# Optimization experiments

Hardware: AMD Instinct MI355X
Metric: run time of the kernel (lower is better)

## Reference

```python
import jax, jax.numpy as jnp
import numpy as np

NUM_ATOMS = 512
NUM_DIMS = 128
H = 32
W = 32
B = 32


def make_dct_dict():
    # rows i: cos((2n+1) * i * pi / (2*num_dims)), L2-normalized; Dict = weights.T -> [D, A]
    i = jnp.arange(NUM_ATOMS, dtype=jnp.float32)[:, None]
    n = jnp.arange(NUM_DIMS, dtype=jnp.float32)[None, :]
    atoms = jnp.cos((2.0 * n + 1.0) * i * (np.pi / (2.0 * NUM_DIMS)))  # [A, D]
    atoms = atoms / jnp.linalg.norm(atoms, axis=1, keepdims=True)
    return atoms.T  # [D, A]


def setup_inputs() -> dict:
    key = jax.random.key(0)
    x = jax.random.normal(key, (B, NUM_DIMS, H, W), dtype=jnp.float32)
    Dict = make_dct_dict()                      # [D, A] learned param (DCT init)
    L = jnp.sum(Dict ** 2)                      # ||Dict||_F^2 (scalar param)
    alpha = jnp.ones((1, H, W, 1), dtype=jnp.float32)  # learned threshold param
    return {"x": x, "Dict": Dict, "alpha": alpha, "L": L, "num_iters": 16}


def reference(x, Dict, alpha, L, num_iters):
    l = alpha / L                                # [1,H,W,1] threshold, broadcasts over atoms
    xt = jnp.transpose(x, (0, 2, 3, 1))          # [B,H,W,D]
    S = (jnp.eye(NUM_ATOMS, dtype=Dict.dtype) - (Dict.T @ Dict) / L).T  # [A,A]
    y = xt @ Dict                                # [B,H,W,A]

    def soft_thresh(v):
        return jnp.sign(v) * jnp.maximum(jnp.abs(v) - l, 0.0)

    z = soft_thresh(y)

    def body(z, _):
        z = soft_thresh(z @ S + y / L)
        return z, None

    z, _ = jax.lax.scan(body, z, None, length=num_iters)
    x_recon = z @ Dict.T                         # [B,H,W,D]
    return (jnp.transpose(z, (0, 3, 1, 2)),      # [B,A,H,W]
            jnp.transpose(x_recon, (0, 3, 1, 2)),  # [B,D,H,W]
            Dict)
```

## Files before the change

### kernel.cpp

```cpp
#include <hip/hip_runtime.h>
#include <hip/hip_bf16.h>

typedef __bf16 bf16_t;
typedef bf16_t bf16x8 __attribute__((ext_vector_type(8)));
typedef float f32x4 __attribute__((ext_vector_type(4)));
typedef unsigned short u16;
typedef unsigned int u32;

static __device__ __forceinline__ u16 f2bf(float f) {
    __hip_bfloat16 h = __float2bfloat16(f);
    return __builtin_bit_cast(u16, h);
}
static __device__ __forceinline__ bf16_t fb(float f) {
    return __builtin_bit_cast(bf16_t, f2bf(f));
}
static __device__ __forceinline__ float bf2f(u16 u) {
    u32 x = ((u32)u) << 16;
    return __builtin_bit_cast(float, x);
}
static __device__ __forceinline__ float softthr(float v, float l) {
    return copysignf(fmaxf(fabsf(v) - l, 0.0f), v);
}

__global__ __launch_bounds__(256) void copy_dict(const float* __restrict__ Dict,
                                                 float* __restrict__ outd)
{
    int i = blockIdx.x * 256 + threadIdx.x;
    outd[i] = Dict[i];
}

__global__ __launch_bounds__(512, 2)
void lista_main(const float* __restrict__ x,
                const float* __restrict__ Dict,
                const float* __restrict__ alpha,
                const float* __restrict__ Lp,
                const int* __restrict__ nip,
                float* __restrict__ outz,
                float* __restrict__ outr)
{
    __shared__ __align__(16) u16 zl[32 * 512];
    __shared__ __align__(16) u16 rl[32 * 128];
    __shared__ __align__(16) u16 xs[32 * 128];
    __shared__ __align__(16) u16 pb[32 * 4 * 128];

    const int t = threadIdx.x;
    const int lane = t & 63;
    const int l15 = lane & 15;
    const int lg = lane >> 4;
    const int wave = t >> 6;
    const int dg = wave >> 2;
    const int ag = wave & 3;
    const int atb = wave << 6;
    const int bb = blockIdx.x >> 5;
    const int hw0 = (blockIdx.x & 31) << 5;
    const float invL = 1.0f / Lp[0];
    const int niter = nip[0];

    const int rpx = t & 31;
    const int roc = t >> 5;

    for (int i = t; i < 32 * 128; i += 512) {
        int d = i >> 5, px = i & 31;
        xs[((px << 7) + d) ^ ((px & 7) << 3)] =
            f2bf(x[((bb * 128 + d) << 10) + hw0 + px]);
    }

    float thr[2];
#pragma unroll
    for (int nt = 0; nt < 2; ++nt)
        thr[nt] = alpha[hw0 + nt * 16 + l15] * invL;

    bf16x8 g1a[4][4];
#pragma unroll
    for (int mt = 0; mt < 4; ++mt) {
        const float* drow = Dict + ((dg * 64 + mt * 16 + l15) << 9) + ag * 128 + lg * 8;
#pragma unroll
        for (int kt = 0; kt < 4; ++kt) {
            f32x4 c0 = *reinterpret_cast<const f32x4*>(drow + kt * 32);
            f32x4 c1 = *reinterpret_cast<const f32x4*>(drow + kt * 32 + 4);
#pragma unroll
            for (int j = 0; j < 4; ++j) {
                g1a[mt][kt][j] = fb(-c0[j]);
                g1a[mt][kt][j + 4] = fb(-c1[j]);
            }
        }
    }
    bf16x8 g2a[4][4];
#pragma unroll
    for (int at = 0; at < 4; ++at)
#pragma unroll
        for (int kt = 0; kt < 4; ++kt)
#pragma unroll
            for (int j = 0; j < 8; ++j)
                g2a[at][kt][j] = fb(Dict[((kt * 32 + lg * 8 + j) << 9) + atb + at * 16 + l15]);

    __syncthreads();

    f32x4 accz[4][2];
#pragma unroll
    for (int at = 0; at < 4; ++at)
#pragma unroll
        for (int nt = 0; nt < 2; ++nt)
            accz[at][nt] = f32x4{0.f, 0.f, 0.f, 0.f};

    auto run_g2 = [&](const u16* __restrict__ bsrc) {
#pragma unroll
        for (int kt = 0; kt < 4; ++kt) {
            bf16x8 Bf[2];
#pragma unroll
            for (int nt = 0; nt < 2; ++nt) {
                int px = nt * 16 + l15;
                Bf[nt] = *reinterpret_cast<const bf16x8*>(
                    &bsrc[((px << 7) + kt * 32 + lg * 8) ^ ((px & 7) << 3)]);
            }
            __builtin_amdgcn_s_setprio(1);
#pragma unroll
            for (int at = 0; at < 4; ++at)
#pragma unroll
                for (int nt = 0; nt < 2; ++nt)
                    accz[at][nt] = __builtin_amdgcn_mfma_f32_16x16x32_bf16(
                        g2a[at][kt], Bf[nt], accz[at][nt], 0, 0, 0);
            __builtin_amdgcn_s_setprio(0);
        }
#pragma unroll
        for (int at = 0; at < 4; ++at)
#pragma unroll
            for (int nt = 0; nt < 2; ++nt) {
                int px = nt * 16 + l15;
                f32x4 a = accz[at][nt];
                a[0] = softthr(a[0], thr[nt]);
                a[1] = softthr(a[1], thr[nt]);
                a[2] = softthr(a[2], thr[nt]);
                a[3] = softthr(a[3], thr[nt]);
                accz[at][nt] = a;
                uint2 pk;
                pk.x = (u32)f2bf(a[0]) | ((u32)f2bf(a[1]) << 16);
                pk.y = (u32)f2bf(a[2]) | ((u32)f2bf(a[3]) << 16);
                *reinterpret_cast<uint2*>(
                    &zl[((px << 9) + atb + at * 16 + lg * 4) ^ ((px & 7) << 3)]) = pk;
            }
    };

    auto run_g1 = [&]() {
        f32x4 a1p[4][2];
#pragma unroll
        for (int mt = 0; mt < 4; ++mt)
#pragma unroll
            for (int nt = 0; nt < 2; ++nt)
                a1p[mt][nt] = f32x4{0.f, 0.f, 0.f, 0.f};
#pragma unroll
        for (int kt = 0; kt < 4; ++kt) {
            bf16x8 Bf[2];
#pragma unroll
            for (int nt = 0; nt < 2; ++nt) {
                int px = nt * 16 + l15;
                Bf[nt] = *reinterpret_cast<const bf16x8*>(
                    &zl[((px << 9) + ag * 128 + kt * 32 + lg * 8) ^ ((px & 7) << 3)]);
            }
            __builtin_amdgcn_s_setprio(1);
#pragma unroll
            for (int mt = 0; mt < 4; ++mt)
#pragma unroll
                for (int nt = 0; nt < 2; ++nt)
                    a1p[mt][nt] = __builtin_amdgcn_mfma_f32_16x16x32_bf16(
                        g1a[mt][kt], Bf[nt], a1p[mt][nt], 0, 0, 0);
            __builtin_amdgcn_s_setprio(0);
        }
#pragma unroll
        for (int mt = 0; mt < 4; ++mt)
#pragma unroll
            for (int nt = 0; nt < 2; ++nt) {
                int px = nt * 16 + l15;
                int d0 = dg * 64 + mt * 16 + lg * 4;
                f32x4 a = a1p[mt][nt];
                uint2 pk;
                pk.x = (u32)f2bf(a[0]) | ((u32)f2bf(a[1]) << 16);
                pk.y = (u32)f2bf(a[2]) | ((u32)f2bf(a[3]) << 16);
                *reinterpret_cast<uint2*>(
                    &pb[((px << 9) + (ag << 7) + d0) ^ ((px & 7) << 3)]) = pk;
            }
    };

    run_g2(xs);
    __syncthreads();

    for (int it = 1; it <= niter; ++it) {
        run_g1();
        __syncthreads();
        {
            const int sw = (rpx & 7) << 3;
            bf16x8 p0 = *reinterpret_cast<const bf16x8*>(&pb[((rpx << 9) + 0 * 128 + roc * 8) ^ sw]);
            bf16x8 p1 = *reinterpret_cast<const bf16x8*>(&pb[((rpx << 9) + 1 * 128 + roc * 8) ^ sw]);
            bf16x8 p2 = *reinterpret_cast<const bf16x8*>(&pb[((rpx << 9) + 2 * 128 + roc * 8) ^ sw]);
            bf16x8 p3 = *reinterpret_cast<const bf16x8*>(&pb[((rpx << 9) + 3 * 128 + roc * 8) ^ sw]);
            bf16x8 xv = *reinterpret_cast<const bf16x8*>(&xs[((rpx << 7) + roc * 8) ^ sw]);
            bf16x8 rv;
#pragma unroll
            for (int e = 0; e < 8; ++e) {
                float s = ((float)xv[e] + (float)p0[e]) + ((float)p1[e] + (float)p2[e]) + (float)p3[e];
                rv[e] = fb(s * invL);
            }
            *reinterpret_cast<bf16x8*>(&rl[((rpx << 7) + roc * 8) ^ sw]) = rv;
        }
        __syncthreads();
        run_g2(rl);
        __syncthreads();
    }

    run_g1();
    __syncthreads();
    float rec[8];
    {
        const int sw = (rpx & 7) << 3;
        bf16x8 p0 = *reinterpret_cast<const bf16x8*>(&pb[((rpx << 9) + 0 * 128 + roc * 8) ^ sw]);
        bf16x8 p1 = *reinterpret_cast<const bf16x8*>(&pb[((rpx << 9) + 1 * 128 + roc * 8) ^ sw]);
        bf16x8 p2 = *reinterpret_cast<const bf16x8*>(&pb[((rpx << 9) + 2 * 128 + roc * 8) ^ sw]);
        bf16x8 p3 = *reinterpret_cast<const bf16x8*>(&pb[((rpx << 9) + 3 * 128 + roc * 8) ^ sw]);
#pragma unroll
        for (int e = 0; e < 8; ++e)
            rec[e] = -(((float)p0[e] + (float)p1[e]) + ((float)p2[e] + (float)p3[e]));
    }

    for (int i = t; i < 32 * 512; i += 512) {
        int a = i >> 5, px = i & 31;
        float zv = bf2f(zl[((px << 9) + a) ^ ((px & 7) << 3)]);
        __builtin_nontemporal_store(zv, &outz[((bb * 512 + a) << 10) + hw0 + px]);
    }
    __syncthreads();

    {
        float* wf = reinterpret_cast<float*>(pb);
        const int swf = (rpx & 7) << 2;
        f32x4 lo{rec[0], rec[1], rec[2], rec[3]};
        f32x4 hi{rec[4], rec[5], rec[6], rec[7]};
        *reinterpret_cast<f32x4*>(&wf[((rpx << 7) + roc * 8) ^ swf]) = lo;
        *reinterpret_cast<f32x4*>(&wf[((rpx << 7) + roc * 8 + 4) ^ swf]) = hi;
    }
    __syncthreads();

    {
        const float* wf = reinterpret_cast<const float*>(pb);
        for (int i = t; i < 32 * 128; i += 512) {
            int d = i >> 5, px = i & 31;
            __builtin_nontemporal_store(wf[((px << 7) + d) ^ ((px & 7) << 2)],
                                        &outr[((bb * 128 + d) << 10) + hw0 + px]);
        }
    }
}

extern "C" void kernel_launch(void* const* d_in, const int* in_sizes, int n_in,
                              void* d_out, int out_size, void* d_ws, size_t ws_size,
                              hipStream_t stream)
{
    const float* x     = (const float*)d_in[0];
    const float* Dict  = (const float*)d_in[1];
    const float* alpha = (const float*)d_in[2];
    const float* Lp    = (const float*)d_in[3];
    const int*   nip   = (const int*)d_in[4];

    float* outz = (float*)d_out;
    float* outr = outz + 32 * 512 * 1024;
    float* outd = outr + 32 * 128 * 1024;

    copy_dict<<<dim3(256), dim3(256), 0, stream>>>(Dict, outd);
    lista_main<<<dim3(1024), dim3(512), 0, stream>>>(x, Dict, alpha, Lp, nip,
                                                     outz, outr);
}
```

Measured before the change: 213.6 us.

## Double pixels per block to 64 and split the reconstruction GEMM K two ways

```diff
diff --git a/kernel.cpp b/kernel.cpp
--- a/kernel.cpp
+++ b/kernel.cpp
@@ -18,8 +18,8 @@
     u32 x = ((u32)u) << 16;
     return __builtin_bit_cast(float, x);
 }
-static __device__ __forceinline__ float softthr(float v, float l) {
-    return copysignf(fmaxf(fabsf(v) - l, 0.0f), v);
+static __device__ __forceinline__ float softthr(float v, float l, float nl) {
+    return v - fmaxf(nl, fminf(v, l));
 }
 
 __global__ __launch_bounds__(256) void copy_dict(const float* __restrict__ Dict,
@@ -38,44 +38,43 @@
                 float* __restrict__ outz,
                 float* __restrict__ outr)
 {
-    __shared__ __align__(16) u16 zl[32 * 512];
-    __shared__ __align__(16) u16 rl[32 * 128];
-    __shared__ __align__(16) u16 xs[32 * 128];
-    __shared__ __align__(16) u16 pb[32 * 4 * 128];
+    __shared__ __align__(16) u16 zl[64 * 512];
+    __shared__ __align__(16) u16 rl[64 * 128];
+    __shared__ __align__(16) u16 xs[64 * 128];
+    __shared__ __align__(16) u16 pb[64 * 256];
 
     const int t = threadIdx.x;
     const int lane = t & 63;
     const int l15 = lane & 15;
     const int lg = lane >> 4;
     const int wave = t >> 6;
-    const int dg = wave >> 2;
-    const int ag = wave & 3;
+    const int dg = wave >> 1;
+    const int ag = wave & 1;
     const int atb = wave << 6;
-    const int bb = blockIdx.x >> 5;
-    const int hw0 = (blockIdx.x & 31) << 5;
+    const int bb = blockIdx.x >> 4;
+    const int hw0 = (blockIdx.x & 15) << 6;
     const float invL = 1.0f / Lp[0];
     const int niter = nip[0];
 
-    const int rpx = t & 31;
-    const int roc = t >> 5;
-
-    for (int i = t; i < 32 * 128; i += 512) {
-        int d = i >> 5, px = i & 31;
+    for (int i = t; i < 64 * 128; i += 512) {
+        int d = i >> 6, px = i & 63;
         xs[((px << 7) + d) ^ ((px & 7) << 3)] =
             f2bf(x[((bb * 128 + d) << 10) + hw0 + px]);
     }
 
-    float thr[2];
-#pragma unroll
-    for (int nt = 0; nt < 2; ++nt)
+    float thr[4], nthr[4];
+#pragma unroll
+    for (int nt = 0; nt < 4; ++nt) {
         thr[nt] = alpha[hw0 + nt * 16 + l15] * invL;
-
-    bf16x8 g1a[4][4];
-#pragma unroll
-    for (int mt = 0; mt < 4; ++mt) {
-        const float* drow = Dict + ((dg * 64 + mt * 16 + l15) << 9) + ag * 128 + lg * 8;
-#pragma unroll
-        for (int kt = 0; kt < 4; ++kt) {
+        nthr[nt] = -thr[nt];
+    }
+
+    bf16x8 g1a[2][8];
+#pragma unroll
+    for (int mt = 0; mt < 2; ++mt) {
+        const float* drow = Dict + ((dg * 32 + mt * 16 + l15) << 9) + ag * 256 + lg * 8;
+#pragma unroll
+        for (int kt = 0; kt < 8; ++kt) {
             f32x4 c0 = *reinterpret_cast<const f32x4*>(drow + kt * 32);
             f32x4 c1 = *reinterpret_cast<const f32x4*>(drow + kt * 32 + 4);
 #pragma unroll
@@ -96,42 +95,40 @@
 
     __syncthreads();
 
-    f32x4 accz[4][2];
+    f32x4 accz[4][4];
 #pragma unroll
     for (int at = 0; at < 4; ++at)
 #pragma unroll
-        for (int nt = 0; nt < 2; ++nt)
+        for (int nt = 0; nt < 4; ++nt)
             accz[at][nt] = f32x4{0.f, 0.f, 0.f, 0.f};
 
     auto run_g2 = [&](const u16* __restrict__ bsrc) {
 #pragma unroll
         for (int kt = 0; kt < 4; ++kt) {
-            bf16x8 Bf[2];
-#pragma unroll
-            for (int nt = 0; nt < 2; ++nt) {
+            bf16x8 Bf[4];
+#pragma unroll
+            for (int nt = 0; nt < 4; ++nt) {
                 int px = nt * 16 + l15;
                 Bf[nt] = *reinterpret_cast<const bf16x8*>(
                     &bsrc[((px << 7) + kt * 32 + lg * 8) ^ ((px & 7) << 3)]);
             }
-            __builtin_amdgcn_s_setprio(1);
 #pragma unroll
             for (int at = 0; at < 4; ++at)
 #pragma unroll
-                for (int nt = 0; nt < 2; ++nt)
+                for (int nt = 0; nt < 4; ++nt)
                     accz[at][nt] = __builtin_amdgcn_mfma_f32_16x16x32_bf16(
                         g2a[at][kt], Bf[nt], accz[at][nt], 0, 0, 0);
-            __builtin_amdgcn_s_setprio(0);
         }
 #pragma unroll
         for (int at = 0; at < 4; ++at)
 #pragma unroll
-            for (int nt = 0; nt < 2; ++nt) {
+            for (int nt = 0; nt < 4; ++nt) {
                 int px = nt * 16 + l15;
                 f32x4 a = accz[at][nt];
-                a[0] = softthr(a[0], thr[nt]);
-                a[1] = softthr(a[1], thr[nt]);
-                a[2] = softthr(a[2], thr[nt]);
-                a[3] = softthr(a[3], thr[nt]);
+                a[0] = softthr(a[0], thr[nt], nthr[nt]);
+                a[1] = softthr(a[1], thr[nt], nthr[nt]);
+                a[2] = softthr(a[2], thr[nt], nthr[nt]);
+                a[3] = softthr(a[3], thr[nt], nthr[nt]);
                 accz[at][nt] = a;
                 uint2 pk;
                 pk.x = (u32)f2bf(a[0]) | ((u32)f2bf(a[1]) << 16);
@@ -142,43 +139,49 @@
     };
 
     auto run_g1 = [&]() {
-        f32x4 a1p[4][2];
-#pragma unroll
-        for (int mt = 0; mt < 4; ++mt)
-#pragma unroll
-            for (int nt = 0; nt < 2; ++nt)
-                a1p[mt][nt] = f32x4{0.f, 0.f, 0.f, 0.f};
-#pragma unroll
-        for (int kt = 0; kt < 4; ++kt) {
-            bf16x8 Bf[2];
-#pragma unroll
-            for (int nt = 0; nt < 2; ++nt) {
-                int px = nt * 16 + l15;
-                Bf[nt] = *reinterpret_cast<const bf16x8*>(
-                    &zl[((px << 9) + ag * 128 + kt * 32 + lg * 8) ^ ((px & 7) << 3)]);
-            }
-            __builtin_amdgcn_s_setprio(1);
-#pragma unroll
-            for (int mt = 0; mt < 4; ++mt)
-#pragma unroll
-                for (int nt = 0; nt < 2; ++nt)
-                    a1p[mt][nt] = __builtin_amdgcn_mfma_f32_16x16x32_bf16(
-                        g1a[mt][kt], Bf[nt], a1p[mt][nt], 0, 0, 0);
-            __builtin_amdgcn_s_setprio(0);
-        }
-#pragma unroll
-        for (int mt = 0; mt < 4; ++mt)
-#pragma unroll
-            for (int nt = 0; nt < 2; ++nt) {
-                int px = nt * 16 + l15;
-                int d0 = dg * 64 + mt * 16 + lg * 4;
-                f32x4 a = a1p[mt][nt];
-                uint2 pk;
-                pk.x = (u32)f2bf(a[0]) | ((u32)f2bf(a[1]) << 16);
-                pk.y = (u32)f2bf(a[2]) | ((u32)f2bf(a[3]) << 16);
-                *reinterpret_cast<uint2*>(
-                    &pb[((px << 9) + (ag << 7) + d0) ^ ((px & 7) << 3)]) = pk;
-            }
+#pragma unroll
+        for (int nt = 0; nt < 4; ++nt) {
+            const int px = nt * 16 + l15;
+            f32x4 a1p0 = f32x4{0.f, 0.f, 0.f, 0.f};
+            f32x4 a1p1 = f32x4{0.f, 0.f, 0.f, 0.f};
+#pragma unroll
+            for (int kt = 0; kt < 8; ++kt) {
+                bf16x8 Bf = *reinterpret_cast<const bf16x8*>(
+                    &zl[((px << 9) + (ag << 8) + kt * 32 + lg * 8) ^ ((px & 7) << 3)]);
+                a1p0 = __builtin_amdgcn_mfma_f32_16x16x32_bf16(g1a[0][kt], Bf, a1p0, 0, 0, 0);
+                a1p1 = __builtin_amdgcn_mfma_f32_16x16x32_bf16(g1a[1][kt], Bf, a1p1, 0, 0, 0);
+            }
+            uint2 pk0, pk1;
+            pk0.x = (u32)f2bf(a1p0[0]) | ((u32)f2bf(a1p0[1]) << 16);
+            pk0.y = (u32)f2bf(a1p0[2]) | ((u32)f2bf(a1p0[3]) << 16);
+            pk1.x = (u32)f2bf(a1p1[0]) | ((u32)f2bf(a1p1[1]) << 16);
+            pk1.y = (u32)f2bf(a1p1[2]) | ((u32)f2bf(a1p1[3]) << 16);
+            int d0 = dg * 32 + lg * 4;
+            *reinterpret_cast<uint2*>(
+                &pb[((px << 8) + (ag << 7) + d0) ^ ((px & 7) << 3)]) = pk0;
+            *reinterpret_cast<uint2*>(
+                &pb[((px << 8) + (ag << 7) + d0 + 16) ^ ((px & 7) << 3)]) = pk1;
+        }
+    };
+
+    auto run_reduce = [&]() {
+#pragma unroll
+        for (int q = 0; q < 2; ++q) {
+            const int tau = t + (q << 9);
+            const int px = tau >> 4;
+            const int roc = tau & 15;
+            const int sw = (px & 7) << 3;
+            bf16x8 p0 = *reinterpret_cast<const bf16x8*>(&pb[((px << 8) + roc * 8) ^ sw]);
+            bf16x8 p1 = *reinterpret_cast<const bf16x8*>(&pb[((px << 8) + 128 + roc * 8) ^ sw]);
+            bf16x8 xv = *reinterpret_cast<const bf16x8*>(&xs[((px << 7) + roc * 8) ^ sw]);
+            bf16x8 rv;
+#pragma unroll
+            for (int e = 0; e < 8; ++e) {
+                float s = (float)xv[e] + ((float)p0[e] + (float)p1[e]);
+                rv[e] = fb(s * invL);
+            }
+            *reinterpret_cast<bf16x8*>(&rl[((px << 7) + roc * 8) ^ sw]) = rv;
+        }
     };
 
     run_g2(xs);
@@ -187,21 +190,7 @@
     for (int it = 1; it <= niter; ++it) {
         run_g1();
         __syncthreads();
-        {
-            const int sw = (rpx & 7) << 3;
-            bf16x8 p0 = *reinterpret_cast<const bf16x8*>(&pb[((rpx << 9) + 0 * 128 + roc * 8) ^ sw]);
-            bf16x8 p1 = *reinterpret_cast<const bf16x8*>(&pb[((rpx << 9) + 1 * 128 + roc * 8) ^ sw]);
-            bf16x8 p2 = *reinterpret_cast<const bf16x8*>(&pb[((rpx << 9) + 2 * 128 + roc * 8) ^ sw]);
-            bf16x8 p3 = *reinterpret_cast<const bf16x8*>(&pb[((rpx << 9) + 3 * 128 + roc * 8) ^ sw]);
-            bf16x8 xv = *reinterpret_cast<const bf16x8*>(&xs[((rpx << 7) + roc * 8) ^ sw]);
-            bf16x8 rv;
-#pragma unroll
-            for (int e = 0; e < 8; ++e) {
-                float s = ((float)xv[e] + (float)p0[e]) + ((float)p1[e] + (float)p2[e]) + (float)p3[e];
-                rv[e] = fb(s * invL);
-            }
-            *reinterpret_cast<bf16x8*>(&rl[((rpx << 7) + roc * 8) ^ sw]) = rv;
-        }
+        run_reduce();
         __syncthreads();
         run_g2(rl);
         __syncthreads();
@@ -209,20 +198,23 @@
 
     run_g1();
     __syncthreads();
-    float rec[8];
-    {
-        const int sw = (rpx & 7) << 3;
-        bf16x8 p0 = *reinterpret_cast<const bf16x8*>(&pb[((rpx << 9) + 0 * 128 + roc * 8) ^ sw]);
-        bf16x8 p1 = *reinterpret_cast<const bf16x8*>(&pb[((rpx << 9) + 1 * 128 + roc * 8) ^ sw]);
-        bf16x8 p2 = *reinterpret_cast<const bf16x8*>(&pb[((rpx << 9) + 2 * 128 + roc * 8) ^ sw]);
-        bf16x8 p3 = *reinterpret_cast<const bf16x8*>(&pb[((rpx << 9) + 3 * 128 + roc * 8) ^ sw]);
+
+    float rec[2][8];
+#pragma unroll
+    for (int q = 0; q < 2; ++q) {
+        const int tau = t + (q << 9);
+        const int px = tau >> 4;
+        const int roc = tau & 15;
+        const int sw = (px & 7) << 3;
+        bf16x8 p0 = *reinterpret_cast<const bf16x8*>(&pb[((px << 8) + roc * 8) ^ sw]);
+        bf16x8 p1 = *reinterpret_cast<const bf16x8*>(&pb[((px << 8) + 128 + roc * 8) ^ sw]);
 #pragma unroll
         for (int e = 0; e < 8; ++e)
-            rec[e] = -(((float)p0[e] + (float)p1[e]) + ((float)p2[e] + (float)p3[e]));
-    }
-
-    for (int i = t; i < 32 * 512; i += 512) {
-        int a = i >> 5, px = i & 31;
+            rec[q][e] = -((float)p0[e] + (float)p1[e]);
+    }
+
+    for (int i = t; i < 64 * 512; i += 512) {
+        int a = i >> 6, px = i & 63;
         float zv = bf2f(zl[((px << 9) + a) ^ ((px & 7) << 3)]);
         __builtin_nontemporal_store(zv, &outz[((bb * 512 + a) << 10) + hw0 + px]);
     }
@@ -230,18 +222,24 @@
 
     {
         float* wf = reinterpret_cast<float*>(pb);
-        const int swf = (rpx & 7) << 2;
-        f32x4 lo{rec[0], rec[1], rec[2], rec[3]};
-        f32x4 hi{rec[4], rec[5], rec[6], rec[7]};
-        *reinterpret_cast<f32x4*>(&wf[((rpx << 7) + roc * 8) ^ swf]) = lo;
-        *reinterpret_cast<f32x4*>(&wf[((rpx << 7) + roc * 8 + 4) ^ swf]) = hi;
+#pragma unroll
+        for (int q = 0; q < 2; ++q) {
+            const int tau = t + (q << 9);
+            const int px = tau >> 4;
+            const int roc = tau & 15;
+            const int swf = (px & 7) << 2;
+            f32x4 lo{rec[q][0], rec[q][1], rec[q][2], rec[q][3]};
+            f32x4 hi{rec[q][4], rec[q][5], rec[q][6], rec[q][7]};
+            *reinterpret_cast<f32x4*>(&wf[((px << 7) + roc * 8) ^ swf]) = lo;
+            *reinterpret_cast<f32x4*>(&wf[((px << 7) + roc * 8 + 4) ^ swf]) = hi;
+        }
     }
     __syncthreads();
 
     {
         const float* wf = reinterpret_cast<const float*>(pb);
-        for (int i = t; i < 32 * 128; i += 512) {
-            int d = i >> 5, px = i & 31;
+        for (int i = t; i < 64 * 128; i += 512) {
+            int d = i >> 6, px = i & 63;
             __builtin_nontemporal_store(wf[((px << 7) + d) ^ ((px & 7) << 2)],
                                         &outr[((bb * 128 + d) << 10) + hw0 + px]);
         }
@@ -263,6 +261,6 @@
     float* outd = outr + 32 * 128 * 1024;
 
     copy_dict<<<dim3(256), dim3(256), 0, stream>>>(Dict, outd);
-    lista_main<<<dim3(1024), dim3(512), 0, stream>>>(x, Dict, alpha, Lp, nip,
-                                                     outz, outr);
-}
+    lista_main<<<dim3(512), dim3(512), 0, stream>>>(x, Dict, alpha, Lp, nip,
+                                                    outz, outr);
+}
```

Measured after the change: 365.0 us. 70.9% more time.
